# Performance work log

Hardware: AMD Instinct MI355X
Metric: run time of the kernel (lower is better)

## Reference

```python
import jax, jax.numpy as jnp
import numpy as np
import math

N_HEADS = 16
LN_EPS = 1e-5


def _layernorm(x, scale, bias):
    mu = jnp.mean(x, axis=-1, keepdims=True)
    var = jnp.var(x, axis=-1, keepdims=True)
    return (x - mu) * jax.lax.rsqrt(var + LN_EPS) * scale + bias


def _pos_encoding(seq_len, d_model, dtype):
    pos = jnp.arange(seq_len, dtype=jnp.float32)[:, None]
    div = jnp.exp(jnp.arange(0, d_model, 2, dtype=jnp.float32) * (-math.log(10000.0) / d_model))
    pe = jnp.zeros((seq_len, d_model), dtype=jnp.float32)
    pe = pe.at[:, 0::2].set(jnp.sin(pos * div))
    pe = pe.at[:, 1::2].set(jnp.cos(pos * div))
    return pe.astype(dtype)


def setup_inputs() -> dict:
    key = jax.random.key(0)
    ks = jax.random.split(key, 8)
    B, S, V, D, L = 2, 1024, 32000, 1024, 6
    F = 4 * D
    sc = 0.02
    return {
        "tokens": jax.random.randint(ks[0], (B, S), 0, V, dtype=jnp.int32),
        "token_emb": jax.random.normal(ks[1], (V, D), jnp.float32) * sc,
        "Wqkv": jax.random.normal(ks[2], (L, D, 3 * D), jnp.float32) * sc,
        "Wout": jax.random.normal(ks[3], (L, D, D), jnp.float32) * sc,
        "ln1_s": jnp.ones((L, D), jnp.float32),
        "ln1_b": jnp.zeros((L, D), jnp.float32),
        "W1": jax.random.normal(ks[4], (L, D, F), jnp.float32) * sc,
        "b1": jnp.zeros((L, F), jnp.float32),
        "W2": jax.random.normal(ks[5], (L, F, D), jnp.float32) * sc,
        "b2": jnp.zeros((L, D), jnp.float32),
        "ln2_s": jnp.ones((L, D), jnp.float32),
        "ln2_b": jnp.zeros((L, D), jnp.float32),
        "lnf_s": jnp.ones((D,), jnp.float32),
        "lnf_b": jnp.zeros((D,), jnp.float32),
        "Whead": jax.random.normal(ks[6], (D, V), jnp.float32) * sc,
        "bhead": jnp.zeros((V,), jnp.float32),
    }


def _forward(tokens, token_emb, Wqkv, Wout, ln1_s, ln1_b, W1, b1, W2, b2,
             ln2_s, ln2_b, lnf_s, lnf_b, Whead, bhead):
    B, S = tokens.shape
    D = token_emb.shape[1]
    L = Wqkv.shape[0]
    H = N_HEADS
    dk = D // H

    x = token_emb[tokens] + _pos_encoding(S, D, token_emb.dtype)  # [B,S,D]
    causal = jnp.tril(jnp.ones((S, S), dtype=bool))
    neg_inf = jnp.finfo(x.dtype).min

    for l in range(L):
        # --- attention sublayer ---
        h = _layernorm(x, ln1_s[l], ln1_b[l])
        qkv = (h @ Wqkv[l]).reshape(B, S, 3, H, dk)
        q, k, v = jnp.moveaxis(qkv, 2, 0)  # each [B,S,H,dk]
        scores = jnp.einsum('bqhd,bkhd->bhqk', q, k) / math.sqrt(dk)
        scores = jnp.where(causal, scores, neg_inf)
        attn = jax.nn.softmax(scores, axis=-1)  # [B,H,S,S]
        o = jnp.einsum('bhqk,bkhd->bqhd', attn, v).reshape(B, S, D)
        x = x + o @ Wout[l]
        # --- FFN sublayer ---
        h2 = _layernorm(x, ln2_s[l], ln2_b[l])
        x = x + jax.nn.gelu(h2 @ W1[l] + b1[l], approximate=False) @ W2[l] + b2[l]

    x = _layernorm(x, lnf_s, lnf_b)
    return x @ Whead + bhead  # [B,S,V]


def reference(tokens, token_emb, Wqkv, Wout, ln1_s, ln1_b, W1, b1, W2, b2,
              ln2_s, ln2_b, lnf_s, lnf_b, Whead, bhead):
    return _forward(tokens, token_emb, Wqkv, Wout, ln1_s, ln1_b, W1, b1, W2, b2,
                    ln2_s, ln2_b, lnf_s, lnf_b, Whead, bhead)
```

## Files before the change

### kernel.cpp

```cpp
#include <hip/hip_runtime.h>
#include <hip/hip_bf16.h>
#include <math.h>

typedef __bf16 bf16;
typedef __bf16 bf16x4 __attribute__((ext_vector_type(4)));
typedef __bf16 bf16x8 __attribute__((ext_vector_type(8)));
typedef float f32x4 __attribute__((ext_vector_type(4)));

#define GL_AS(p) ((const __attribute__((address_space(1))) void*)(p))
#define LDS_AS(p) ((__attribute__((address_space(3))) void*)(p))

__device__ inline void xcd_remap(int& bm, int& bn, int NBM, int NBN)
{
    const int nwg = NBM * NBN;
    const int flat = bm + NBM * bn;
    const int q = nwg >> 3, r = nwg & 7;
    const int x = flat & 7, i = flat >> 3;
    const int f2 = ((x < r) ? x * (q + 1) : r * (q + 1) + (x - r) * q) + i;
    bm = f2 % NBM;
    bn = f2 / NBM;
}

struct TSeg {
    const float* in; bf16* out; int R, C, nTilesC, tilesPerZ, nTiles;
};

__global__ __launch_bounds__(256) void transpose_all_k(
    TSeg s0, TSeg s1, TSeg s2, TSeg s3, TSeg s4)
{
    int t = blockIdx.x;
    TSeg s;
    if (t < s0.nTiles) s = s0;
    else { t -= s0.nTiles;
    if (t < s1.nTiles) s = s1;
    else { t -= s1.nTiles;
    if (t < s2.nTiles) s = s2;
    else { t -= s2.nTiles;
    if (t < s3.nTiles) s = s3;
    else { t -= s3.nTiles; s = s4; }}}}

    const int z   = t / s.tilesPerZ;
    const int rem = t - z * s.tilesPerZ;
    const int cx  = rem % s.nTilesC, ry = rem / s.nTilesC;

    __shared__ float tl[32][33];
    const int c0 = cx * 32, r0 = ry * 32;
    const size_t zoff = (size_t)z * s.R * s.C;
    const float* inb = s.in + zoff;
    bf16* outb = s.out + zoff;
    const int tx = threadIdx.x, ty = threadIdx.y;
#pragma unroll
    for (int i = 0; i < 32; i += 8)
        tl[ty + i][tx] = inb[(size_t)(r0 + ty + i) * s.C + c0 + tx];
    __syncthreads();
#pragma unroll
    for (int i = 0; i < 32; i += 8)
        outb[(size_t)(c0 + ty + i) * s.R + r0 + tx] = (bf16)tl[tx][ty + i];
}

__global__ __launch_bounds__(256) void embed_k(
    const int* __restrict__ tok, const float* __restrict__ emb,
    float* __restrict__ x)
{
    const int D = 1024;
    const int row = blockIdx.x;
    const int s = row & 1023;
    const int t = tok[row];
    const int d0 = threadIdx.x * 4;
    const float c = 9.210340371976184f / 512.0f;
    const float div0 = expf(-(float)(d0 >> 1) * c);
    const float div1 = expf(-(float)((d0 >> 1) + 1) * c);
    const float a0 = (float)s * div0, a1 = (float)s * div1;
    const f32x4 e = *(const f32x4*)(emb + (size_t)t * D + d0);
    f32x4 o;
    o[0] = e[0] + sinf(a0);
    o[1] = e[1] + cosf(a0);
    o[2] = e[2] + sinf(a1);
    o[3] = e[3] + cosf(a1);
    *(f32x4*)(x + (size_t)row * D + d0) = o;
}

__global__ __launch_bounds__(256) void layernorm_k(
    const float* __restrict__ x, const float* __restrict__ sc,
    const float* __restrict__ bi, bf16* __restrict__ out)
{
    const int D = 1024;
    const int row = blockIdx.x;
    const int d0 = threadIdx.x * 4;
    const f32x4 v = *(const f32x4*)(x + (size_t)row * D + d0);
    float s = v[0] + v[1] + v[2] + v[3];
    float q = v[0] * v[0] + v[1] * v[1] + v[2] * v[2] + v[3] * v[3];
#pragma unroll
    for (int o = 32; o; o >>= 1) { s += __shfl_xor(s, o); q += __shfl_xor(q, o); }
    __shared__ float ls[4], lq[4];
    const int w = threadIdx.x >> 6;
    if ((threadIdx.x & 63) == 0) { ls[w] = s; lq[w] = q; }
    __syncthreads();
    const float S = ls[0] + ls[1] + ls[2] + ls[3];
    const float Q = lq[0] + lq[1] + lq[2] + lq[3];
    const float mu = S * (1.0f / D);
    const float var = Q * (1.0f / D) - mu * mu;
    const float rstd = rsqrtf(var + 1e-5f);
    const f32x4 sc4 = *(const f32x4*)(sc + d0);
    const f32x4 bi4 = *(const f32x4*)(bi + d0);
    bf16x4 o4;
#pragma unroll
    for (int i = 0; i < 4; ++i) o4[i] = (bf16)((v[i] - mu) * rstd * sc4[i] + bi4[i]);
    *(bf16x4*)(out + (size_t)row * D + d0) = o4;
}

template <int EPI, int SK = 1, bool SWZ = true>
__global__ __launch_bounds__(256, 2) void gemm_bt_k(
    const bf16* __restrict__ A, const bf16* __restrict__ Bt,
    float* __restrict__ Cf, bf16* __restrict__ Cb, bf16* __restrict__ Cb2,
    const float* __restrict__ bias, int M, int N, int K)
{
    __shared__ __align__(16) bf16 Al[128 * 64];
    __shared__ __align__(16) bf16 Bl[128 * 64];
    const int tid = threadIdx.x;
    const int l = tid & 63;
    const int wbase = tid & 192;
    const int wr = (tid >> 7) & 1, wc = (tid >> 6) & 1;
    int bm = blockIdx.x, bn = blockIdx.y;
    if constexpr (SWZ) xcd_remap(bm, bn, gridDim.x, gridDim.y);
    const int kz = blockIdx.z;
    const int Kc = K / SK;

    f32x4 acc[4][4];
#pragma unroll
    for (int i = 0; i < 4; ++i)
#pragma unroll
        for (int j = 0; j < 4; ++j) acc[i][j] = (f32x4){0.f, 0.f, 0.f, 0.f};

    const bf16* Abase = A + (size_t)bm * 128 * K + (size_t)kz * Kc;
    const bf16* Bbase = Bt + (size_t)bn * 128 * K + (size_t)kz * Kc;

    for (int k0 = 0; k0 < Kc; k0 += 64) {
#pragma unroll
        for (int i = 0; i < 4; ++i) {
            const int c = i * 256 + tid;
            const int row = c >> 3, slot = c & 7;
            const int col = ((slot ^ (row & 7)) << 3);
            __builtin_amdgcn_global_load_lds(
                GL_AS(Abase + (size_t)row * K + k0 + col),
                LDS_AS(Al + (i * 256 + wbase) * 8), 16, 0, 0);
        }
#pragma unroll
        for (int i = 0; i < 4; ++i) {
            const int c = i * 256 + tid;
            const int row = c >> 3, slot = c & 7;
            const int col = ((slot ^ (row & 7)) << 3);
            __builtin_amdgcn_global_load_lds(
                GL_AS(Bbase + (size_t)row * K + k0 + col),
                LDS_AS(Bl + (i * 256 + wbase) * 8), 16, 0, 0);
        }
        __syncthreads();

#pragma unroll
        for (int ks = 0; ks < 2; ++ks) {
            bf16x8 af[4], bfr[4];
            const int kb = ks * 64 + ((l >> 4) << 4);
#pragma unroll
            for (int mi = 0; mi < 4; ++mi) {
                const int r = wr * 64 + mi * 16 + (l & 15);
                af[mi] = *(const bf16x8*)((const char*)Al + r * 128 + (kb ^ ((r & 7) << 4)));
            }
#pragma unroll
            for (int ni = 0; ni < 4; ++ni) {
                const int r = wc * 64 + ni * 16 + (l & 15);
                bfr[ni] = *(const bf16x8*)((const char*)Bl + r * 128 + (kb ^ ((r & 7) << 4)));
            }
#pragma unroll
            for (int mi = 0; mi < 4; ++mi)
#pragma unroll
                for (int ni = 0; ni < 4; ++ni)
                    acc[mi][ni] = __builtin_amdgcn_mfma_f32_16x16x32_bf16(
                        af[mi], bfr[ni], acc[mi][ni], 0, 0, 0);
        }
        __syncthreads();
    }

    const int colb = bn * 128 + wc * 64;
    const int rowb = bm * 128 + wr * 64 + ((l >> 4) << 2);
#pragma unroll
    for (int mi = 0; mi < 4; ++mi) {
#pragma unroll
        for (int ni = 0; ni < 4; ++ni) {
            const int col = colb + ni * 16 + (l & 15);
            if constexpr (EPI == 5) {
                const int row0 = rowb + mi * 16;
                if (col < 2048) {
#pragma unroll
                    for (int j = 0; j < 4; ++j)
                        Cb[(size_t)(row0 + j) * N + col] = (bf16)acc[mi][ni][j];
                } else {
                    bf16x4 v4;
#pragma unroll
                    for (int j = 0; j < 4; ++j) v4[j] = (bf16)acc[mi][ni][j];
                    *(bf16x4*)&Cb2[((size_t)(row0 >> 3) * 1024 + (col - 2048)) * 8 + (row0 & 7)] = v4;
                }
            } else {
#pragma unroll
                for (int j = 0; j < 4; ++j) {
                    const int row = rowb + mi * 16 + j;
                    const float v = acc[mi][ni][j];
                    if constexpr (EPI == 0) {
                        Cb[(size_t)row * N + col] = (bf16)v;
                    } else if constexpr (EPI == 1) {
                        if constexpr (SK > 1) atomicAdd(&Cf[(size_t)row * N + col], v);
                        else                  Cf[(size_t)row * N + col] += v;
                    } else if constexpr (EPI == 2) {
                        const float u = v + bias[col];
                        const float g = 0.5f * u * (1.0f + erff(u * 0.70710678118654752f));
                        Cb[(size_t)row * N + col] = (bf16)g;
                    } else if constexpr (EPI == 3) {
                        const float add = (SK == 1 || kz == 0) ? v + bias[col] : v;
                        if constexpr (SK > 1) atomicAdd(&Cf[(size_t)row * N + col], add);
                        else                  Cf[(size_t)row * N + col] += add;
                    } else if constexpr (EPI == 4) {
                        Cf[(size_t)row * N + col] = v + bias[col];
                    }
                }
            }
        }
    }
}

__global__ __launch_bounds__(256) void attn_mfma_k(
    const bf16* __restrict__ qkv, const bf16* __restrict__ vt,
    bf16* __restrict__ o)
{
    __shared__ __align__(16) bf16 Kl[2][64 * 64];
    __shared__ __align__(16) bf16 Vl[2][64 * 64];
    __shared__ __align__(16) bf16 Pl[4][16][136];

    const int tid = threadIdx.x;
    const int w = tid >> 6, l = tid & 63;
    const int g = l >> 4, lc = l & 15;
    const int bh = blockIdx.x >> 4;
    int qt = blockIdx.x & 15;
    if (bh & 16) qt = 15 - qt;
    const int h = bh & 15, b = bh >> 4;
    const int q0 = qt * 64;
    const int qw = q0 + w * 16;
    const int NT = qt + 1;

    const bf16* qbase = qkv + (size_t)b * 1024 * 3072 + h * 64;
    const bf16* kbase = qbase + 1024;
    const bf16* vbase = vt + (size_t)b * 128 * 8192 + h * 512;

    bf16x8 af0, af1;
    {
        const bf16* qp = qbase + (size_t)(qw + lc) * 3072 + g * 8;
        af0 = *(const bf16x8*)qp;
        af1 = *(const bf16x8*)(qp + 32);
    }

    f32x4 acc[4];
#pragma unroll
    for (int dt = 0; dt < 4; ++dt) acc[dt] = (f32x4){0.f, 0.f, 0.f, 0.f};
    f32x4 m  = (f32x4){-1e30f, -1e30f, -1e30f, -1e30f};
    f32x4 ls = (f32x4){0.f, 0.f, 0.f, 0.f};

    auto stage = [&](int t) {
        const int k0 = t * 64;
        const int buf = t & 1;
#pragma unroll
        for (int ld = 0; ld < 2; ++ld) {
            const int c = ld * 256 + tid;
            const int row = c >> 3;
            const int d = (((c & 7) ^ (row & 7)) << 3);
            __builtin_amdgcn_global_load_lds(
                GL_AS(kbase + (size_t)(k0 + row) * 3072 + d),
                LDS_AS(Kl[buf] + (ld * 256 + (tid & 192)) * 8), 16, 0, 0);
        }
#pragma unroll
        for (int ld = 0; ld < 2; ++ld) {
            const int c = ld * 256 + tid;
            const int row = c >> 3;
            const int so = (c & 7) ^ (row & 7);
            __builtin_amdgcn_global_load_lds(
                GL_AS(vbase + (size_t)((k0 >> 3) + so) * 8192 + row * 8),
                LDS_AS(Vl[buf] + (ld * 256 + (tid & 192)) * 8), 16, 0, 0);
        }
    };

    auto compute = [&](int t, bool MASKED) {
        const char* KT = (const char*)Kl[t & 1];
        const char* VT = (const char*)Vl[t & 1];
        const int k0 = t * 64;

        f32x4 s[4];
#pragma unroll
        for (int kt = 0; kt < 4; ++kt) {
            const int r = kt * 16 + lc;
            const bf16x8 kf0 = *(const bf16x8*)(KT + r * 128 + ((g * 16)      ^ ((r & 7) << 4)));
            const bf16x8 kf1 = *(const bf16x8*)(KT + r * 128 + ((64 + g * 16) ^ ((r & 7) << 4)));
            f32x4 sv = (f32x4){0.f, 0.f, 0.f, 0.f};
            sv = __builtin_amdgcn_mfma_f32_16x16x32_bf16(af0, kf0, sv, 0, 0, 0);
            sv = __builtin_amdgcn_mfma_f32_16x16x32_bf16(af1, kf1, sv, 0, 0, 0);
            s[kt] = sv;
        }

#pragma unroll
        for (int kt = 0; kt < 4; ++kt)
#pragma unroll
            for (int j = 0; j < 4; ++j) {
                if (MASKED) {
                    const int row = qw + 4 * g + j;
                    s[kt][j] = (k0 + kt * 16 + lc <= row) ? s[kt][j] * 0.125f : -1e30f;
                } else {
                    s[kt][j] *= 0.125f;
                }
            }

        f32x4 tm;
#pragma unroll
        for (int j = 0; j < 4; ++j)
            tm[j] = fmaxf(fmaxf(s[0][j], s[1][j]), fmaxf(s[2][j], s[3][j]));
#pragma unroll
        for (int off = 8; off; off >>= 1)
#pragma unroll
            for (int j = 0; j < 4; ++j) tm[j] = fmaxf(tm[j], __shfl_xor(tm[j], off));

        f32x4 sc;
#pragma unroll
        for (int j = 0; j < 4; ++j) {
            const float mn = fmaxf(m[j], tm[j]);
            sc[j] = __expf(m[j] - mn);
            m[j] = mn;
        }
        f32x4 p[4];
#pragma unroll
        for (int kt = 0; kt < 4; ++kt)
#pragma unroll
            for (int j = 0; j < 4; ++j) p[kt][j] = __expf(s[kt][j] - m[j]);
#pragma unroll
        for (int j = 0; j < 4; ++j)
            ls[j] = ls[j] * sc[j] + ((p[0][j] + p[1][j]) + (p[2][j] + p[3][j]));
#pragma unroll
        for (int dt = 0; dt < 4; ++dt)
#pragma unroll
            for (int j = 0; j < 4; ++j) acc[dt][j] *= sc[j];

#pragma unroll
        for (int j = 0; j < 4; ++j) {
            const int r = 4 * g + j;
#pragma unroll
            for (int kt = 0; kt < 4; ++kt) {
                const bf16 hi = (bf16)p[kt][j];
                Pl[w][r][kt * 16 + lc]      = hi;
                Pl[w][r][72 + kt * 16 + lc] = (bf16)(p[kt][j] - (float)hi);
            }
        }
        bf16x8 pah[2], pal[2];
#pragma unroll
        for (int ks = 0; ks < 2; ++ks) {
            pah[ks] = *(const bf16x8*)&Pl[w][lc][ks * 32 + g * 8];
            pal[ks] = *(const bf16x8*)&Pl[w][lc][72 + ks * 32 + g * 8];
        }

#pragma unroll
        for (int dt = 0; dt < 4; ++dt) {
            const int r = dt * 16 + lc;
            const bf16x8 vf0 = *(const bf16x8*)(VT + r * 128 + ((g * 16)      ^ ((r & 7) << 4)));
            const bf16x8 vf1 = *(const bf16x8*)(VT + r * 128 + ((64 + g * 16) ^ ((r & 7) << 4)));
            f32x4 a = acc[dt];
            a = __builtin_amdgcn_mfma_f32_16x16x32_bf16(pah[0], vf0, a, 0, 0, 0);
            a = __builtin_amdgcn_mfma_f32_16x16x32_bf16(pah[1], vf1, a, 0, 0, 0);
            a = __builtin_amdgcn_mfma_f32_16x16x32_bf16(pal[0], vf0, a, 0, 0, 0);
            a = __builtin_amdgcn_mfma_f32_16x16x32_bf16(pal[1], vf1, a, 0, 0, 0);
            acc[dt] = a;
        }
    };

    stage(0);
    __syncthreads();
    for (int t = 0; t < NT; ++t) {
        if (t + 1 < NT) stage(t + 1);
        compute(t, t == NT - 1);
        __syncthreads();
    }

    f32x4 inv;
#pragma unroll
    for (int j = 0; j < 4; ++j) {
        float s = ls[j];
#pragma unroll
        for (int off = 8; off; off >>= 1) s += __shfl_xor(s, off);
        inv[j] = 1.0f / s;
    }
    bf16* op = o + (size_t)(b * 1024 + qw) * 1024 + h * 64;
#pragma unroll
    for (int dt = 0; dt < 4; ++dt)
#pragma unroll
        for (int j = 0; j < 4; ++j)
            op[(size_t)(4 * g + j) * 1024 + dt * 16 + lc] = (bf16)(acc[dt][j] * inv[j]);
}

extern "C" void kernel_launch(void* const* d_in, const int* in_sizes, int n_in,
                              void* d_out, int out_size, void* d_ws, size_t ws_size,
                              hipStream_t stream)
{
    const int B = 2, S = 1024, D = 1024, L = 6, F = 4096, V = 32000, H = 16;
    const int M = B * S;

    const int*   tokens    = (const int*)  d_in[0];
    const float* token_emb = (const float*)d_in[1];
    const float* Wqkv      = (const float*)d_in[2];
    const float* Wout      = (const float*)d_in[3];
    const float* ln1_s     = (const float*)d_in[4];
    const float* ln1_b     = (const float*)d_in[5];
    const float* W1        = (const float*)d_in[6];
    const float* b1        = (const float*)d_in[7];
    const float* W2        = (const float*)d_in[8];
    const float* b2        = (const float*)d_in[9];
    const float* ln2_s     = (const float*)d_in[10];
    const float* ln2_b     = (const float*)d_in[11];
    const float* lnf_s     = (const float*)d_in[12];
    const float* lnf_b     = (const float*)d_in[13];
    const float* Whead     = (const float*)d_in[14];
    const float* bhead     = (const float*)d_in[15];
    float* out = (float*)d_out;

    char* w = (char*)d_ws;
    size_t off = 0;
    auto alloc = [&](size_t n) { char* p = w + off; off += (n + 255) & ~(size_t)255; return p; };
    bf16* WqkvT  = (bf16*)alloc((size_t)L * 3 * D * D * 2);
    bf16* WoutT  = (bf16*)alloc((size_t)L * D * D * 2);
    bf16* W1T    = (bf16*)alloc((size_t)L * F * D * 2);
    bf16* W2T    = (bf16*)alloc((size_t)L * D * F * 2);
    bf16* WheadT = (bf16*)alloc((size_t)V * D * 2);
    float* x     = (float*)alloc((size_t)M * D * 4);
    bf16* h      = (bf16*)alloc((size_t)M * D * 2);
    bf16* qkv    = (bf16*)alloc((size_t)M * 3 * D * 2);
    bf16* ob     = (bf16*)alloc((size_t)M * D * 2);
    bf16* mid    = (bf16*)alloc((size_t)M * F * 2);
    bf16* vt     = mid;

    TSeg s0{Wqkv,  WqkvT,  D, 3 * D, 3 * D / 32, (3 * D / 32) * (D / 32), (3 * D / 32) * (D / 32) * L};
    TSeg s1{Wout,  WoutT,  D, D,     D / 32,     (D / 32) * (D / 32),     (D / 32) * (D / 32) * L};
    TSeg s2{W1,    W1T,    D, F,     F / 32,     (F / 32) * (D / 32),     (F / 32) * (D / 32) * L};
    TSeg s3{W2,    W2T,    F, D,     D / 32,     (D / 32) * (F / 32),     (D / 32) * (F / 32) * L};
    TSeg s4{Whead, WheadT, D, V,     V / 32,     (V / 32) * (D / 32),     (V / 32) * (D / 32)};
    const int totTiles = s0.nTiles + s1.nTiles + s2.nTiles + s3.nTiles + s4.nTiles;
    transpose_all_k<<<totTiles, dim3(32, 8), 0, stream>>>(s0, s1, s2, s3, s4);

    embed_k<<<M, 256, 0, stream>>>(tokens, token_emb, x);

    for (int lyr = 0; lyr < L; ++lyr) {
        layernorm_k<<<M, 256, 0, stream>>>(x, ln1_s + lyr * D, ln1_b + lyr * D, h);
        gemm_bt_k<5><<<dim3(M / 128, 3 * D / 128), 256, 0, stream>>>(
            h, WqkvT + (size_t)lyr * 3 * D * D, nullptr, qkv, vt, nullptr, M, 3 * D, D);
        attn_mfma_k<<<B * H * S / 64, 256, 0, stream>>>(qkv, vt, ob);
        gemm_bt_k<1, 2><<<dim3(M / 128, D / 128, 2), 256, 0, stream>>>(
            ob, WoutT + (size_t)lyr * D * D, x, nullptr, nullptr, nullptr, M, D, D);
        layernorm_k<<<M, 256, 0, stream>>>(x, ln2_s + lyr * D, ln2_b + lyr * D, h);
        gemm_bt_k<2><<<dim3(M / 128, F / 128), 256, 0, stream>>>(
            h, W1T + (size_t)lyr * F * D, nullptr, mid, nullptr, b1 + lyr * F, M, F, D);
        gemm_bt_k<3, 2><<<dim3(M / 128, D / 128, 2), 256, 0, stream>>>(
            mid, W2T + (size_t)lyr * D * F, x, nullptr, nullptr, b2 + lyr * D, M, D, F);
    }
    layernorm_k<<<M, 256, 0, stream>>>(x, lnf_s, lnf_b, h);
    gemm_bt_k<4, 1, false><<<dim3(M / 128, V / 128), 256, 0, stream>>>(
        h, WheadT, out, nullptr, nullptr, bhead, M, V, D);
}
```

Before: 1.445 ms.

## Use exp2 softmax, pack P hi/lo in LDS, and split LM head GEMM into slices

The attention softmax now folds log2(e) into the score scale and calls exp2f instead of __expf. The hi/lo bf16 split of P is packed into 32-bit words in one LDS array and unpacked with bit operations, which changes the LDS store pattern. The final vocabulary projection is issued as four column-slice launches with a column offset instead of one large grid, probably to change cache locality or scheduling. This adds launch overhead and extra ALU work for unpacking.

```diff
diff --git a/kernel.cpp b/kernel.cpp
--- a/kernel.cpp
+++ b/kernel.cpp
@@ -6,6 +6,7 @@
 typedef __bf16 bf16x4 __attribute__((ext_vector_type(4)));
 typedef __bf16 bf16x8 __attribute__((ext_vector_type(8)));
 typedef float f32x4 __attribute__((ext_vector_type(4)));
+typedef unsigned int u32x4 __attribute__((ext_vector_type(4)));
 
 #define GL_AS(p) ((const __attribute__((address_space(1))) void*)(p))
 #define LDS_AS(p) ((__attribute__((address_space(3))) void*)(p))
@@ -113,7 +114,7 @@
 __global__ __launch_bounds__(256, 2) void gemm_bt_k(
     const bf16* __restrict__ A, const bf16* __restrict__ Bt,
     float* __restrict__ Cf, bf16* __restrict__ Cb, bf16* __restrict__ Cb2,
-    const float* __restrict__ bias, int M, int N, int K)
+    const float* __restrict__ bias, int M, int N, int K, int bn0)
 {
     __shared__ __align__(16) bf16 Al[128 * 64];
     __shared__ __align__(16) bf16 Bl[128 * 64];
@@ -180,7 +181,7 @@
         __syncthreads();
     }
 
-    const int colb = bn * 128 + wc * 64;
+    const int colb = (bn0 + bn) * 128 + wc * 64;
     const int rowb = bm * 128 + wr * 64 + ((l >> 4) << 2);
 #pragma unroll
     for (int mi = 0; mi < 4; ++mi) {
@@ -232,7 +233,7 @@
 {
     __shared__ __align__(16) bf16 Kl[2][64 * 64];
     __shared__ __align__(16) bf16 Vl[2][64 * 64];
-    __shared__ __align__(16) bf16 Pl[4][16][136];
+    __shared__ __align__(16) unsigned int Pp[4][16][76];
 
     const int tid = threadIdx.x;
     const int w = tid >> 6, l = tid & 63;
@@ -285,6 +286,8 @@
         }
     };
 
+    const float SCL = 0.18033688011112042f;
+
     auto compute = [&](int t, bool MASKED) {
         const char* KT = (const char*)Kl[t & 1];
         const char* VT = (const char*)Vl[t & 1];
@@ -308,9 +311,9 @@
             for (int j = 0; j < 4; ++j) {
                 if (MASKED) {
                     const int row = qw + 4 * g + j;
-                    s[kt][j] = (k0 + kt * 16 + lc <= row) ? s[kt][j] * 0.125f : -1e30f;
+                    s[kt][j] = (k0 + kt * 16 + lc <= row) ? s[kt][j] * SCL : -1e30f;
                 } else {
-                    s[kt][j] *= 0.125f;
+                    s[kt][j] *= SCL;
                 }
             }
 
@@ -327,14 +330,14 @@
 #pragma unroll
         for (int j = 0; j < 4; ++j) {
             const float mn = fmaxf(m[j], tm[j]);
-            sc[j] = __expf(m[j] - mn);
+            sc[j] = exp2f(m[j] - mn);
             m[j] = mn;
         }
         f32x4 p[4];
 #pragma unroll
         for (int kt = 0; kt < 4; ++kt)
 #pragma unroll
-            for (int j = 0; j < 4; ++j) p[kt][j] = __expf(s[kt][j] - m[j]);
+            for (int j = 0; j < 4; ++j) p[kt][j] = exp2f(s[kt][j] - m[j]);
 #pragma unroll
         for (int j = 0; j < 4; ++j)
             ls[j] = ls[j] * sc[j] + ((p[0][j] + p[1][j]) + (p[2][j] + p[3][j]));
@@ -348,16 +351,30 @@
             const int r = 4 * g + j;
 #pragma unroll
             for (int kt = 0; kt < 4; ++kt) {
-                const bf16 hi = (bf16)p[kt][j];
-                Pl[w][r][kt * 16 + lc]      = hi;
-                Pl[w][r][72 + kt * 16 + lc] = (bf16)(p[kt][j] - (float)hi);
+                const bf16 hb = (bf16)p[kt][j];
+                const bf16 lb = (bf16)(p[kt][j] - (float)hb);
+                Pp[w][r][kt * 16 + lc] =
+                    (unsigned)__builtin_bit_cast(unsigned short, hb) |
+                    ((unsigned)__builtin_bit_cast(unsigned short, lb) << 16);
             }
         }
         bf16x8 pah[2], pal[2];
 #pragma unroll
         for (int ks = 0; ks < 2; ++ks) {
-            pah[ks] = *(const bf16x8*)&Pl[w][lc][ks * 32 + g * 8];
-            pal[ks] = *(const bf16x8*)&Pl[w][lc][72 + ks * 32 + g * 8];
+            const unsigned* prow = &Pp[w][lc][ks * 32 + g * 8];
+            const u32x4 ca = *(const u32x4*)prow;
+            const u32x4 cb = *(const u32x4*)(prow + 4);
+            u32x4 hh, ll;
+            hh[0] = (ca[0] & 0xffffu) | (ca[1] << 16);
+            hh[1] = (ca[2] & 0xffffu) | (ca[3] << 16);
+            hh[2] = (cb[0] & 0xffffu) | (cb[1] << 16);
+            hh[3] = (cb[2] & 0xffffu) | (cb[3] << 16);
+            ll[0] = (ca[0] >> 16) | (ca[1] & 0xffff0000u);
+            ll[1] = (ca[2] >> 16) | (ca[3] & 0xffff0000u);
+            ll[2] = (cb[0] >> 16) | (cb[1] & 0xffff0000u);
+            ll[3] = (cb[2] >> 16) | (cb[3] & 0xffff0000u);
+            pah[ks] = __builtin_bit_cast(bf16x8, hh);
+            pal[ks] = __builtin_bit_cast(bf16x8, ll);
         }
 
 #pragma unroll
@@ -451,17 +468,25 @@
     for (int lyr = 0; lyr < L; ++lyr) {
         layernorm_k<<<M, 256, 0, stream>>>(x, ln1_s + lyr * D, ln1_b + lyr * D, h);
         gemm_bt_k<5><<<dim3(M / 128, 3 * D / 128), 256, 0, stream>>>(
-            h, WqkvT + (size_t)lyr * 3 * D * D, nullptr, qkv, vt, nullptr, M, 3 * D, D);
+            h, WqkvT + (size_t)lyr * 3 * D * D, nullptr, qkv, vt, nullptr, M, 3 * D, D, 0);
         attn_mfma_k<<<B * H * S / 64, 256, 0, stream>>>(qkv, vt, ob);
         gemm_bt_k<1, 2><<<dim3(M / 128, D / 128, 2), 256, 0, stream>>>(
-            ob, WoutT + (size_t)lyr * D * D, x, nullptr, nullptr, nullptr, M, D, D);
+            ob, WoutT + (size_t)lyr * D * D, x, nullptr, nullptr, nullptr, M, D, D, 0);
         layernorm_k<<<M, 256, 0, stream>>>(x, ln2_s + lyr * D, ln2_b + lyr * D, h);
         gemm_bt_k<2><<<dim3(M / 128, F / 128), 256, 0, stream>>>(
-            h, W1T + (size_t)lyr * F * D, nullptr, mid, nullptr, b1 + lyr * F, M, F, D);
+            h, W1T + (size_t)lyr * F * D, nullptr, mid, nullptr, b1 + lyr * F, M, F, D, 0);
         gemm_bt_k<3, 2><<<dim3(M / 128, D / 128, 2), 256, 0, stream>>>(
-            mid, W2T + (size_t)lyr * D * F, x, nullptr, nullptr, b2 + lyr * D, M, D, F);
+            mid, W2T + (size_t)lyr * D * F, x, nullptr, nullptr, b2 + lyr * D, M, D, F, 0);
     }
     layernorm_k<<<M, 256, 0, stream>>>(x, lnf_s, lnf_b, h);
-    gemm_bt_k<4, 1, false><<<dim3(M / 128, V / 128), 256, 0, stream>>>(
-        h, WheadT, out, nullptr, nullptr, bhead, M, V, D);
-}
+    {
+        const int slice[4] = {63, 63, 62, 62};
+        int n0 = 0;
+        for (int si = 0; si < 4; ++si) {
+            gemm_bt_k<4, 1, false><<<dim3(M / 128, slice[si]), 256, 0, stream>>>(
+                h, WheadT + (size_t)n0 * 128 * D, out, nullptr, nullptr, bhead,
+                M, V, D, n0);
+            n0 += slice[si];
+        }
+    }
+}
```

Result: slower. 1.509 ms (+4.4%).
